# Performance work log

Hardware: AMD Instinct MI355X
Metric: run time of the kernel (lower is better)

## Reference

```python
import jax, jax.numpy as jnp
import numpy as np

B, M, N = 16, 64, 64
F = 64
H2 = 2 * F
L = 2
OUT1, OUT2, PREDS = 32, 32, 256


def skew(x):
    # (b,m,n,c) -> (b,m,m+n-1,c); row i shifted right by i
    b, m, n, c = x.shape
    pad = jnp.pad(x, ((0, 0), (0, 0), (0, m - 1), (0, 0)))
    return jax.vmap(lambda row, r: jnp.roll(row, r, axis=1), in_axes=(1, 0), out_axes=1)(pad, jnp.arange(m))


def unskew(x):
    b, m, n2, c = x.shape
    n = n2 - m + 1
    un = jax.vmap(lambda row, r: jnp.roll(row, -r, axis=1), in_axes=(1, 0), out_axes=1)(x, jnp.arange(m))
    return un[:, :, :n]


def _ln(x, s, b, eps=1e-6):
    mu = jnp.mean(x, axis=-1, keepdims=True)
    var = jnp.mean(jnp.square(x - mu), axis=-1, keepdims=True)
    return (x - mu) * jax.lax.rsqrt(var + eps) * s + b


def _diag_layer(xin, lns, lnb, wis, bis, wss, bss, woc, boc, h0p):
    # xin: (b,m,n2,2F); scan over diagonals (n2 axis)
    b, m, n2, h2 = xin.shape
    f = h2 // 2

    def step(carry, xt):  # xt: (b,m,2F)
        h, c = carry
        xn = _ln(xt, lns, lnb)
        # is_kernel: 1x1 conv == linear; ss_kernel: causal k=2 conv along m
        hprev = jnp.pad(h, ((0, 0), (1, 0), (0, 0)))[:, :-1]
        z = xn @ wis + bis + hprev @ wss[0] + h @ wss[1] + bss  # (b,m,4F)
        fg, ig, og, gg = jnp.split(z, 4, axis=-1)
        cn = jax.nn.sigmoid(fg) * c + jax.nn.sigmoid(ig) * jnp.tanh(gg)
        hn = jax.nn.sigmoid(og) * jnp.tanh(cn)
        x_out = hn @ woc + boc + xn  # residual uses post-LN x (as in source)
        return (hn, cn), x_out

    h0t = jnp.broadcast_to(h0p, (b, m, f))  # h0p: (1,F)
    c0 = jnp.zeros((b, m, f), xin.dtype)
    _, out = jax.lax.scan(step, (h0t, c0), xin.transpose(2, 0, 1, 3))
    return out.transpose(1, 2, 0, 3)


def _forward(im, conv_in_k, conv_in_b, ln_s, ln_b, w_is, b_is, w_ss, b_ss,
             w_oc, b_oc, h0, w_out1, b_out1, w_out2, b_out2, w_head, b_head):
    # mask-A for the 7x7 input conv
    mask = jnp.ones(conv_in_k.shape, conv_in_k.dtype)
    mask = mask.at[3:, 4:].set(0.0)
    mask = mask.at[4:].set(0.0)
    mask = mask.at[3, 3].set(0.0)
    x = skew(im)  # (b,m,n2,1)
    x = jax.lax.conv_general_dilated(x, conv_in_k * mask, (1, 1), 'SAME',
                                     dimension_numbers=('NHWC', 'HWIO', 'NHWC')) + conv_in_b
    b, m, n2, h2 = x.shape
    for l in range(ln_s.shape[0]):
        left = _diag_layer(x, ln_s[l, 0], ln_b[l, 0], w_is[l, 0], b_is[l, 0],
                           w_ss[l, 0], b_ss[l, 0], w_oc[l, 0], b_oc[l, 0], h0[l, 0])
        right = _diag_layer(x[:, :, ::-1, :], ln_s[l, 1], ln_b[l, 1], w_is[l, 1], b_is[l, 1],
                            w_ss[l, 1], b_ss[l, 1], w_oc[l, 1], b_oc[l, 1], h0[l, 1])[:, :, ::-1, :]
        right = jnp.concatenate([jnp.zeros((b, 1, n2, h2), x.dtype), right[:, :-1]], axis=1)
        x = left + right
    x = unskew(x)  # (b,m,n,2F)
    x = x @ w_out1 + b_out1
    x = x @ w_out2 + b_out2
    return x @ w_head + b_head  # (b,m,n,256)


def setup_inputs() -> dict:
    key = jax.random.key(0)
    ks = jax.random.split(key, 10)
    rn = lambda k, s: jax.random.normal(k, s, jnp.float32) * 0.05
    return {
        "im": jax.random.uniform(ks[0], (B, M, N, 1), jnp.float32),
        "conv_in_k": rn(ks[1], (7, 7, 1, H2)),
        "conv_in_b": jnp.zeros((H2,), jnp.float32),
        "ln_s": jnp.ones((L, 2, H2), jnp.float32),
        "ln_b": jnp.zeros((L, 2, H2), jnp.float32),
        "w_is": rn(ks[2], (L, 2, H2, 4 * F)),
        "b_is": jnp.zeros((L, 2, 4 * F), jnp.float32),
        "w_ss": rn(ks[3], (L, 2, 2, F, 4 * F)),
        "b_ss": jnp.zeros((L, 2, 4 * F), jnp.float32),
        "w_oc": rn(ks[4], (L, 2, F, H2)),
        "b_oc": jnp.zeros((L, 2, H2), jnp.float32),
        "h0": rn(ks[5], (L, 2, 1, F)),
        "w_out1": rn(ks[6], (H2, OUT1)),
        "b_out1": jnp.zeros((OUT1,), jnp.float32),
        "w_out2": rn(ks[7], (OUT1, OUT2)),
        "b_out2": jnp.zeros((OUT2,), jnp.float32),
        "w_head": rn(ks[8], (OUT2, PREDS)),
        "b_head": jnp.zeros((PREDS,), jnp.float32),
    }


def reference(im, conv_in_k, conv_in_b, ln_s, ln_b, w_is, b_is, w_ss, b_ss,
              w_oc, b_oc, h0, w_out1, b_out1, w_out2, b_out2, w_head, b_head):
    return _forward(im, conv_in_k, conv_in_b, ln_s, ln_b, w_is, b_is, w_ss, b_ss,
                    w_oc, b_oc, h0, w_out1, b_out1, w_out2, b_out2, w_head, b_head)
```

## Files before the change

### kernel.cpp

```cpp
#include <hip/hip_runtime.h>

typedef unsigned short ushort_t;
typedef unsigned int uint_t;
typedef __attribute__((ext_vector_type(8))) short s8bf;
typedef __attribute__((ext_vector_type(4))) float f32x4;

#define N2 127
#define ACT ((size_t)16*64*127*128)
#define HNE ((size_t)16*64*127*64)
#define MBW ((size_t)32*3*127*64)

__device__ inline float bf_lo(uint_t v){ return __uint_as_float(v << 16); }
__device__ inline float bf_hi(uint_t v){ return __uint_as_float(v & 0xffff0000u); }
__device__ inline ushort_t f2bf(float f){
  uint_t u = __float_as_uint(f);
  uint_t r = ((u >> 16) & 1u) + 0x7fffu;
  return (ushort_t)((u + r) >> 16);
}
__device__ inline float bf2f(ushort_t h){ return __uint_as_float(((uint_t)h) << 16); }
__device__ inline float frcp(float x){ return __builtin_amdgcn_rcpf(x); }
__device__ inline float sigm(float x){ return frcp(1.f + __expf(-x)); }
__device__ inline float tanhf_(float x){
  float e = __expf(2.f * x);
  return 1.f - 2.f * frcp(1.f + e);
}
__device__ inline void unpack8(uint4 u, float* x){
  x[0]=bf_lo(u.x); x[1]=bf_hi(u.x); x[2]=bf_lo(u.y); x[3]=bf_hi(u.y);
  x[4]=bf_lo(u.z); x[5]=bf_hi(u.z); x[6]=bf_lo(u.w); x[7]=bf_hi(u.w);
}
__device__ inline f32x4 zero4(){ f32x4 v; v[0]=0.f; v[1]=0.f; v[2]=0.f; v[3]=0.f; return v; }
__device__ inline f32x4 splat4(float s){ f32x4 v; v[0]=s; v[1]=s; v[2]=s; v[3]=s; return v; }

__device__ inline void rowstats(const float* xr, float& mu, float& rstd){
  float s0=0.f, q0=0.f;
#pragma unroll
  for (int k = 0; k < 32; k++){ s0 += xr[k]; q0 += xr[k]*xr[k]; }
  s0 += __shfl_xor(s0, 1); q0 += __shfl_xor(q0, 1);
  s0 += __shfl_xor(s0, 2); q0 += __shfl_xor(q0, 2);
  mu = s0 * 0.0078125f;
  float var = q0 * 0.0078125f - mu*mu;
  rstd = rsqrtf(var + 1e-6f);
}

__global__ void pack_kernel(const float* __restrict__ w_is, const float* __restrict__ w_ss,
                            const float* __restrict__ b_is, const float* __restrict__ b_ss,
                            const float* __restrict__ w_oc, const float* __restrict__ w1,
                            const float* __restrict__ w2, const float* __restrict__ wh,
                            const float* __restrict__ ck,
                            ushort_t* __restrict__ zWp, ushort_t* __restrict__ wisp,
                            ushort_t* __restrict__ wocp,
                            float* __restrict__ zbias, float* __restrict__ w1T,
                            float* __restrict__ w2T, float* __restrict__ whT,
                            float* __restrict__ kw, uint_t* __restrict__ mb)
{
  int idx = blockIdx.x * 256 + threadIdx.x;
  if (idx < 131072){
    int ld = idx >> 15; int r = idx & 32767;
    int e = r & 7, lane = (r >> 3) & 63, ctg = (r >> 9) & 15, kk = r >> 13;
    int k = kk*32 + ((lane >> 4) & 3)*8 + e;
    int n = ctg*16 + (lane & 15);
    float v;
    if (k < 64) v = w_ss[(((size_t)ld*2 + 0)*64 + k)*256 + n];
    else        v = w_ss[(((size_t)ld*2 + 1)*64 + (k-64))*256 + n];
    zWp[idx] = f2bf(v);
  } else if (idx < 262144){
    int r0 = idx - 131072;
    int ld = r0 >> 15; int r = r0 & 32767;
    int e = r & 7, lane = (r >> 3) & 63, ctg = (r >> 9) & 15, kk = r >> 13;
    int k = kk*32 + ((lane >> 4) & 3)*8 + e;
    int n = ctg*16 + (lane & 15);
    wisp[r0] = f2bf(w_is[((size_t)ld*128 + k)*256 + n]);
  } else if (idx < 294912){
    int r0 = idx - 262144;
    int ld = r0 >> 13; int r = r0 & 8191;
    int e = r & 7, lane = (r >> 3) & 63, ctg = (r >> 9) & 7, kk = (r >> 12) & 1;
    int k = kk*32 + ((lane >> 4) & 3)*8 + e;
    int n = ctg*16 + (lane & 15);
    wocp[r0] = f2bf(w_oc[((size_t)ld*64 + k)*128 + n]);
  } else if (idx < 295936){
    int r = idx - 294912;
    zbias[r] = b_is[r] + b_ss[r];
  } else if (idx < 300032){
    int r = idx - 295936;
    int c = r >> 7, k = r & 127;
    w1T[r] = w1[k*32 + c];
  } else if (idx < 301056){
    int r = idx - 300032;
    int c = r >> 5, k = r & 31;
    w2T[r] = w2[k*32 + c];
  } else if (idx < 309248){
    int r = idx - 301056;
    int o = r >> 5, k = r & 31;
    whT[r] = wh[k*256 + o];
  } else if (idx < 312320){
    int r = idx - 309248;
    int tau = r >> 7, ch = r & 127;
    int di, dj;
    if (tau < 21){ di = tau/7 - 3; dj = tau%7 - 3; } else { di = 0; dj = tau - 24; }
    kw[r] = ck[((di+3)*7 + (dj+3))*128 + ch];
  } else if (idx < (int)(312320 + MBW)){
    mb[idx - 312320] = 0u;
  }
}

__global__ __launch_bounds__(256) void conv_kernel(const float* __restrict__ im,
                const float* __restrict__ cb, const float* __restrict__ kw,
                ushort_t* __restrict__ out)
{
  int tid = threadIdx.x;
  int p = blockIdx.x*2 + (tid >> 7);
  int ch = tid & 127;
  int b = p / (64*N2); int rem = p - b*(64*N2);
  int i = rem / N2; int j = rem - i*N2;
  int base = j - i;
  float acc = cb[ch];
#pragma unroll
  for (int tau = 0; tau < 24; tau++){
    int di = (tau < 21) ? (tau/7 - 3) : 0;
    int dj = (tau < 21) ? (tau%7 - 3) : (tau - 24);
    int ii = i + di;
    int jx = base + dj - di;
    if (ii >= 0 && jx >= 0 && jx < 64)
      acc += im[(b*64 + ii)*64 + jx] * kw[tau*128 + ch];
  }
  out[(size_t)p*128 + ch] = f2bf(acc);
}

__device__ inline void write_frags(const ushort_t* __restrict__ XN,
                                   ushort_t* __restrict__ dst, int tid){
  int lane = tid & 63, kkq = tid >> 6;
  int quad = (lane >> 4) & 3, l16 = lane & 15;
#pragma unroll
  for (int rt = 0; rt < 4; rt++){
    uint4 v = *(const uint4*)&XN[(size_t)(rt*16 + l16)*136 + kkq*32 + quad*8];
    *(uint4*)(dst + (size_t)((kkq*4 + rt)*64 + lane)*8) = v;
  }
}

__device__ inline void ln_to_XN(ushort_t* __restrict__ XN, int row, int lq,
                                const float* xr, float mu, float rstd,
                                const float* __restrict__ ln_s,
                                const float* __restrict__ ln_b, int ld){
#pragma unroll
  for (int k = 0; k < 32; k++){
    int c = lq*32 + k;
    float xn = (xr[k] - mu)*rstd*ln_s[ld*128 + c] + ln_b[ld*128 + c];
    XN[(size_t)row*136 + c] = f2bf(xn);
  }
}

__global__ __launch_bounds__(256, 2) void stage_kernel(
    int mode, int woclyr, int lnlyr,
    ushort_t* __restrict__ Xbuf,
    const ushort_t* __restrict__ hnL, const ushort_t* __restrict__ hnR,
    const ushort_t* __restrict__ wocp, const float* __restrict__ b_oc,
    const float* __restrict__ ln_s, const float* __restrict__ ln_b,
    ushort_t* __restrict__ xnfL, ushort_t* __restrict__ xnfR)
{
  __shared__ __align__(16) float Xout[64*132];
  __shared__ __align__(16) ushort_t XN[64*136];
  __shared__ __align__(16) ushort_t XNh[64*72];

  const int tid = threadIdx.x;
  const int bj = blockIdx.x;
  const int b = bj / 127, j = bj - b*127;
  const int w = tid >> 6, lane = tid & 63, quad = (lane >> 4) & 3, l16 = lane & 15;
  const int row = tid >> 2, lq = tid & 3;

  float xr[32];
  {
    const uint4* p = (const uint4*)(Xbuf + ((size_t)(b*64 + row)*N2 + j)*128 + lq*32);
    unpack8(p[0], xr); unpack8(p[1], xr+8); unpack8(p[2], xr+16); unpack8(p[3], xr+24);
  }
  float mu, rstd;
  rowstats(xr, mu, rstd);

  if (mode == 0){
    ln_to_XN(XN, row, lq, xr, mu, rstd, ln_s, ln_b, lnlyr*2 + 0);
    __syncthreads();
    write_frags(XN, xnfL + (size_t)bj*8192, tid);
    __syncthreads();
    ln_to_XN(XN, row, lq, xr, mu, rstd, ln_s, ln_b, lnlyr*2 + 1);
    __syncthreads();
    write_frags(XN, xnfR + (size_t)bj*8192, tid);
    return;
  }

#pragma unroll 1
  for (int s = 0; s < 2; s++){
    const int ld = woclyr*2 + s;
    ln_to_XN(XN, row, lq, xr, mu, rstd, ln_s, ln_b, ld);
    {
      const ushort_t* hp = s ? hnR : hnL;
      const uint4* p = (const uint4*)(hp + ((size_t)(b*64 + row)*N2 + j)*64 + lq*16);
      *(uint4*)&XNh[(size_t)row*72 + lq*16]     = p[0];
      *(uint4*)&XNh[(size_t)row*72 + lq*16 + 8] = p[1];
    }
    __syncthreads();
    s8bf bw[2][2];
#pragma unroll
    for (int kk = 0; kk < 2; kk++)
#pragma unroll
      for (int jt = 0; jt < 2; jt++)
        bw[kk][jt] = *(const s8bf*)(wocp + (size_t)ld*8192 + (size_t)(((kk*8 + (2*w + jt))*64 + lane)*8));
    f32x4 a2[4][2];
#pragma unroll
    for (int rt = 0; rt < 4; rt++){ a2[rt][0] = zero4(); a2[rt][1] = zero4(); }
#pragma unroll
    for (int kk = 0; kk < 2; kk++)
#pragma unroll
      for (int rt = 0; rt < 4; rt++){
        s8bf a = *(const s8bf*)&XNh[(size_t)(rt*16 + l16)*72 + kk*32 + quad*8];
#pragma unroll
        for (int jt = 0; jt < 2; jt++)
          a2[rt][jt] = __builtin_amdgcn_mfma_f32_16x16x32_bf16(a, bw[kk][jt], a2[rt][jt], 0, 0, 0);
      }
    const float bv0 = b_oc[ld*128 + 32*w + l16];
    const float bv1 = b_oc[ld*128 + 32*w + 16 + l16];
#pragma unroll
    for (int rt = 0; rt < 4; rt++)
#pragma unroll
      for (int jt = 0; jt < 2; jt++){
        int col = 32*w + 16*jt + l16;
        float bv = jt ? bv1 : bv0;
#pragma unroll
        for (int r = 0; r < 4; r++){
          int rr = rt*16 + quad*4 + r;
          float v = a2[rt][jt][r] + bv + bf2f(XN[(size_t)rr*136 + col]);
          if (s == 0) Xout[(size_t)rr*132 + col] = v;
          else if (rr < 63) Xout[(size_t)(rr + 1)*132 + col] += v;
        }
      }
    __syncthreads();
  }

  float xo[32];
#pragma unroll
  for (int k = 0; k < 32; k++) xo[k] = Xout[(size_t)row*132 + lq*32 + k];
  {
    uint_t o[16];
#pragma unroll
    for (int k = 0; k < 16; k++){
      ushort_t lo = f2bf(xo[2*k]);
      ushort_t hi = f2bf(xo[2*k + 1]);
      o[k] = (uint_t)lo | ((uint_t)hi << 16);
    }
    uint4* dst = (uint4*)(Xbuf + ((size_t)(b*64 + row)*N2 + j)*128 + lq*32);
#pragma unroll
    for (int q2 = 0; q2 < 4; q2++) dst[q2] = make_uint4(o[q2*4], o[q2*4+1], o[q2*4+2], o[q2*4+3]);
  }
  if (mode == 2) return;

  float mu2, rstd2;
  rowstats(xo, mu2, rstd2);
  ln_to_XN(XN, row, lq, xo, mu2, rstd2, ln_s, ln_b, lnlyr*2 + 0);
  __syncthreads();
  write_frags(XN, xnfL + (size_t)bj*8192, tid);
  __syncthreads();
  ln_to_XN(XN, row, lq, xo, mu2, rstd2, ln_s, ln_b, lnlyr*2 + 1);
  __syncthreads();
  write_frags(XN, xnfR + (size_t)bj*8192, tid);
}

__global__ __launch_bounds__(256, 1) void diag_kernel(
    const ushort_t* __restrict__ xnfL, const ushort_t* __restrict__ xnfR,
    ushort_t* __restrict__ hnL, ushort_t* __restrict__ hnR,
    const ushort_t* __restrict__ zWp, const ushort_t* __restrict__ wisp,
    const float* __restrict__ zbias, const float* __restrict__ h0, int layer,
    uint_t* __restrict__ mb)
{
  __shared__ ushort_t A[2][16][136];

  const int tid = threadIdx.x;
  const int g = blockIdx.x & 3;
  const int b = (blockIdx.x >> 2) & 15;
  const int d = blockIdx.x >> 6;
  const int ld = layer*2 + d;
  const ushort_t* xnf = d ? xnfR : xnfL;
  ushort_t* hp = d ? hnR : hnL;

  const int w = tid >> 6;
  const int lane = tid & 63;
  const int quad = lane >> 4;
  const int l16 = lane & 15;
  const int cg = w*16 + l16;

  s8bf bss[4][4], bis[4][4];
#pragma unroll
  for (int kk = 0; kk < 4; kk++)
#pragma unroll
    for (int ct = 0; ct < 4; ct++){
      size_t fo = (size_t)(((kk*16 + (w + 4*ct))*64 + lane)*8);
      bss[kk][ct] = *(const s8bf*)(zWp  + (size_t)ld*32768 + fo);
      bis[kk][ct] = *(const s8bf*)(wisp + (size_t)ld*32768 + fo);
    }
  float zb[4];
#pragma unroll
  for (int ct = 0; ct < 4; ct++) zb[ct] = zbias[ld*256 + ct*64 + cg];

  float c_reg[4] = {0.f, 0.f, 0.f, 0.f};

  {
    int r2 = tid >> 4, q8 = tid & 15;
    const float* h0p = h0 + ld*64;
#pragma unroll
    for (int k = 0; k < 8; k++){
      int c = q8*8 + k;
      ushort_t hb = f2bf(h0p[c & 63]);
      ushort_t v;
      if (c < 64) v = (g == 0 && r2 == 0) ? (ushort_t)0 : hb;
      else        v = hb;
      A[0][r2][c] = v;
      A[1][r2][c] = v;
    }
  }

  const int stp8 = d ? -8192 : 8192;
  const ushort_t* xbase = xnf + ((size_t)b*127 + (d ? 126 : 0))*8192;
  uint4 xf[4];
#pragma unroll
  for (int kk = 0; kk < 4; kk++)
    xf[kk] = *(const uint4*)(xbase + (size_t)((kk*4 + g)*64 + lane)*8);

  f32x4 acc[4];
#pragma unroll
  for (int ct = 0; ct < 4; ct++) acc[ct] = splat4(zb[ct]);
#pragma unroll
  for (int kk = 0; kk < 4; kk++){
    s8bf a = *(const s8bf*)&xf[kk];
#pragma unroll
    for (int ct = 0; ct < 4; ct++)
      acc[ct] = __builtin_amdgcn_mfma_f32_16x16x32_bf16(a, bis[kk][ct], acc[ct], 0, 0, 0);
  }
  const ushort_t* pfp = xbase + stp8;
#pragma unroll
  for (int kk = 0; kk < 4; kk++)
    xf[kk] = *(const uint4*)(pfp + (size_t)((kk*4 + g)*64 + lane)*8);
  pfp += stp8;

  const int dj64 = d ? -64 : 64;
  ushort_t* hlane = hp + ((size_t)(b*64 + g*16 + quad*4)*N2 + (d ? 126 : 0))*64 + cg;

  const int bd = b*2 + d;
  uint_t* mbOut = mb + ((size_t)(bd*3 + g)*127)*64;
  const uint_t* mbIn = mb + ((size_t)(bd*3 + (g > 0 ? g - 1 : 0))*127)*64;
  const uint_t stampBase = (uint_t)layer * 127u;
  const bool isProd = (g < 3);
  const bool isCons = (g > 0) && (w == 1);

  __syncthreads();

#pragma unroll 1
  for (int t = 0; t < 127; t++){
    const int pr = t & 1, pn = pr ^ 1;
    const uint_t stamp = stampBase + (uint_t)t + 1u;
    const bool doFetch = isCons && (t < 126);

    uint_t pv = 0;
    if (doFetch)
      pv = __hip_atomic_load(mbIn + (size_t)t*64 + lane,
                             __ATOMIC_RELAXED, __HIP_MEMORY_SCOPE_AGENT);

#pragma unroll
    for (int kk = 0; kk < 4; kk++){
      s8bf af = *(const s8bf*)&A[pr][l16][kk*32 + quad*8];
#pragma unroll
      for (int ct = 0; ct < 4; ct++)
        acc[ct] = __builtin_amdgcn_mfma_f32_16x16x32_bf16(af, bss[kk][ct], acc[ct], 0, 0, 0);
    }

#pragma unroll
    for (int r = 0; r < 4; r++){
      float fg = sigm(acc[0][r]);
      float ig = sigm(acc[1][r]);
      float og = sigm(acc[2][r]);
      float gg = tanhf_(acc[3][r]);
      float cn = fg*c_reg[r] + ig*gg;
      c_reg[r] = cn;
      float hn = og * tanhf_(cn);
      int rr = quad*4 + r;
      ushort_t hb = f2bf(hn);
      A[pn][rr][64 + cg] = hb;
      if (rr < 15) A[pn][rr + 1][cg] = hb;
      hlane[(size_t)r*8128] = hb;
      if (r == 3 && isProd && quad == 3 && t < 126)
        __hip_atomic_store(mbOut + (size_t)t*64 + cg,
                           (stamp << 16) | (uint_t)hb,
                           __ATOMIC_RELAXED, __HIP_MEMORY_SCOPE_AGENT);
    }
    hlane += dj64;

    if (t < 126){
#pragma unroll
      for (int ct = 0; ct < 4; ct++) acc[ct] = splat4(zb[ct]);
#pragma unroll
      for (int kk = 0; kk < 4; kk++){
        s8bf a = *(const s8bf*)&xf[kk];
#pragma unroll
        for (int ct = 0; ct < 4; ct++)
          acc[ct] = __builtin_amdgcn_mfma_f32_16x16x32_bf16(a, bis[kk][ct], acc[ct], 0, 0, 0);
      }
      if (t < 125){
#pragma unroll
        for (int kk = 0; kk < 4; kk++)
          xf[kk] = *(const uint4*)(pfp + (size_t)((kk*4 + g)*64 + lane)*8);
        pfp += stp8;
      }
    }

    if (doFetch){
      while (!__all((pv >> 16) == stamp))
        pv = __hip_atomic_load(mbIn + (size_t)t*64 + lane,
                               __ATOMIC_RELAXED, __HIP_MEMORY_SCOPE_AGENT);
      A[pn][0][lane] = (ushort_t)(pv & 0xffffu);
    }

    __syncthreads();
  }
}

__global__ __launch_bounds__(256) void head_kernel(
    const ushort_t* __restrict__ xfin,
    const float* __restrict__ w1T, const float* __restrict__ b1,
    const float* __restrict__ w2T, const float* __restrict__ b2,
    const float* __restrict__ whT, const float* __restrict__ bh,
    float* __restrict__ out)
{
  __shared__ float xf[64][132];
  __shared__ float v1[64][36];
  __shared__ float v2[64][36];
  int tid = threadIdx.x;
  int b = blockIdx.x >> 6, i = blockIdx.x & 63;
  {
    int jj = tid >> 2, q = tid & 3;
    size_t base = ((size_t)(b*64 + i)*N2 + (i + jj))*128 + q*32;
    const uint4* pL = (const uint4*)(xfin + base);
    float x[32];
    unpack8(pL[0], x); unpack8(pL[1], x+8); unpack8(pL[2], x+16); unpack8(pL[3], x+24);
#pragma unroll
    for (int k = 0; k < 32; k++) xf[jj][q*32 + k] = x[k];
  }
  __syncthreads();
  {
    int c1 = tid & 31, jg = tid >> 5;
    float wr[128];
    const float4* wp = (const float4*)(w1T + c1*128);
#pragma unroll
    for (int kk = 0; kk < 32; kk++) ((float4*)wr)[kk] = wp[kk];
#pragma unroll 1
    for (int jj2 = 0; jj2 < 8; jj2++){
      int jr = jg*8 + jj2;
      float a0=0.f,a1=0.f,a2=0.f,a3=0.f;
#pragma unroll
      for (int kk = 0; kk < 32; kk++){
        float4 xv = *(const float4*)&xf[jr][kk*4];
        a0 += xv.x*wr[kk*4]; a1 += xv.y*wr[kk*4+1]; a2 += xv.z*wr[kk*4+2]; a3 += xv.w*wr[kk*4+3];
      }
      v1[jr][c1] = b1[c1] + (a0+a1)+(a2+a3);
    }
  }
  __syncthreads();
  {
    int c2 = tid & 31, jg = tid >> 5;
    float wr[32];
    const float4* wp = (const float4*)(w2T + c2*32);
#pragma unroll
    for (int kk = 0; kk < 8; kk++) ((float4*)wr)[kk] = wp[kk];
#pragma unroll 1
    for (int jj2 = 0; jj2 < 8; jj2++){
      int jr = jg*8 + jj2;
      float a0=0.f,a1=0.f,a2=0.f,a3=0.f;
#pragma unroll
      for (int kk = 0; kk < 8; kk++){
        float4 xv = *(const float4*)&v1[jr][kk*4];
        a0 += xv.x*wr[kk*4]; a1 += xv.y*wr[kk*4+1]; a2 += xv.z*wr[kk*4+2]; a3 += xv.w*wr[kk*4+3];
      }
      v2[jr][c2] = b2[c2] + (a0+a1)+(a2+a3);
    }
  }
  __syncthreads();
  {
    int o = tid;
    float wr[32];
    const float4* wp = (const float4*)(whT + o*32);
#pragma unroll
    for (int kk = 0; kk < 8; kk++) ((float4*)wr)[kk] = wp[kk];
    float bo = bh[o];
#pragma unroll 1
    for (int jr = 0; jr < 64; jr++){
      float a0=0.f,a1=0.f,a2=0.f,a3=0.f;
#pragma unroll
      for (int kk = 0; kk < 8; kk++){
        float4 xv = *(const float4*)&v2[jr][kk*4];
        a0 += xv.x*wr[kk*4]; a1 += xv.y*wr[kk*4+1]; a2 += xv.z*wr[kk*4+2]; a3 += xv.w*wr[kk*4+3];
      }
      out[(((size_t)b*64 + i)*64 + jr)*256 + o] = bo + (a0+a1)+(a2+a3);
    }
  }
}

extern "C" void kernel_launch(void* const* d_in, const int* in_sizes, int n_in,
                              void* d_out, int out_size, void* d_ws, size_t ws_size,
                              hipStream_t stream)
{
  const float* im   = (const float*)d_in[0];
  const float* ck   = (const float*)d_in[1];
  const float* cb   = (const float*)d_in[2];
  const float* ln_s = (const float*)d_in[3];
  const float* ln_b = (const float*)d_in[4];
  const float* w_is = (const float*)d_in[5];
  const float* b_is = (const float*)d_in[6];
  const float* w_ss = (const float*)d_in[7];
  const float* b_ss = (const float*)d_in[8];
  const float* w_oc = (const float*)d_in[9];
  const float* b_oc = (const float*)d_in[10];
  const float* h0   = (const float*)d_in[11];
  const float* w1   = (const float*)d_in[12];
  const float* b1   = (const float*)d_in[13];
  const float* w2   = (const float*)d_in[14];
  const float* b2   = (const float*)d_in[15];
  const float* wh   = (const float*)d_in[16];
  const float* bh   = (const float*)d_in[17];

  ushort_t* Xbuf = (ushort_t*)d_ws;
  ushort_t* xnfL = Xbuf + ACT;
  ushort_t* xnfR = xnfL + ACT;
  ushort_t* hnL  = xnfR + ACT;
  ushort_t* hnR  = hnL + HNE;
  ushort_t* zWp  = hnR + HNE;
  ushort_t* wisp = zWp + 131072;
  ushort_t* wocp = wisp + 131072;
  float* zbias = (float*)(wocp + 32768);
  float* w1T   = zbias + 1024;
  float* w2T   = w1T + 4096;
  float* whT   = w2T + 1024;
  float* kw    = whT + 8192;
  uint_t* mb   = (uint_t*)d_out;

  pack_kernel<<<4268, 256, 0, stream>>>(w_is, w_ss, b_is, b_ss, w_oc, w1, w2, wh, ck,
                                        zWp, wisp, wocp, zbias, w1T, w2T, whT, kw, mb);
  conv_kernel<<<65024, 256, 0, stream>>>(im, cb, kw, Xbuf);
  stage_kernel<<<2032, 256, 0, stream>>>(0, 0, 0, Xbuf, nullptr, nullptr,
                                         wocp, b_oc, ln_s, ln_b, xnfL, xnfR);
  diag_kernel<<<128, 256, 0, stream>>>(xnfL, xnfR, hnL, hnR, zWp, wisp, zbias, h0, 0, mb);
  stage_kernel<<<2032, 256, 0, stream>>>(1, 0, 1, Xbuf, hnL, hnR,
                                         wocp, b_oc, ln_s, ln_b, xnfL, xnfR);
  diag_kernel<<<128, 256, 0, stream>>>(xnfL, xnfR, hnL, hnR, zWp, wisp, zbias, h0, 1, mb);
  stage_kernel<<<2032, 256, 0, stream>>>(2, 1, 0, Xbuf, hnL, hnR,
                                         wocp, b_oc, ln_s, ln_b, xnfL, xnfR);
  head_kernel<<<1024, 256, 0, stream>>>(Xbuf, w1T, b1, w2T, b2, whT, bh, (float*)d_out);
}
```

Before: 793.6 us.

## Merge both scan directions into one 512-thread diag block and deepen prefetch

```diff
diff --git a/kernel.cpp b/kernel.cpp
--- a/kernel.cpp
+++ b/kernel.cpp
@@ -262,24 +262,25 @@
   write_frags(XN, xnfR + (size_t)bj*8192, tid);
 }
 
-__global__ __launch_bounds__(256, 1) void diag_kernel(
+__global__ __launch_bounds__(512, 1) void diag_kernel(
     const ushort_t* __restrict__ xnfL, const ushort_t* __restrict__ xnfR,
     ushort_t* __restrict__ hnL, ushort_t* __restrict__ hnR,
     const ushort_t* __restrict__ zWp, const ushort_t* __restrict__ wisp,
     const float* __restrict__ zbias, const float* __restrict__ h0, int layer,
     uint_t* __restrict__ mb)
 {
-  __shared__ ushort_t A[2][16][136];
+  __shared__ ushort_t A[2][2][16][136];
 
   const int tid = threadIdx.x;
   const int g = blockIdx.x & 3;
-  const int b = (blockIdx.x >> 2) & 15;
-  const int d = blockIdx.x >> 6;
+  const int b = blockIdx.x >> 2;
+  const int w8 = tid >> 6;
+  const int d = w8 >> 2;
+  const int w = w8 & 3;
   const int ld = layer*2 + d;
   const ushort_t* xnf = d ? xnfR : xnfL;
   ushort_t* hp = d ? hnR : hnL;
 
-  const int w = tid >> 6;
   const int lane = tid & 63;
   const int quad = lane >> 4;
   const int l16 = lane & 15;
@@ -301,7 +302,8 @@
   float c_reg[4] = {0.f, 0.f, 0.f, 0.f};
 
   {
-    int r2 = tid >> 4, q8 = tid & 15;
+    int t8 = tid & 255;
+    int r2 = t8 >> 4, q8 = t8 & 15;
     const float* h0p = h0 + ld*64;
 #pragma unroll
     for (int k = 0; k < 8; k++){
@@ -310,33 +312,41 @@
       ushort_t v;
       if (c < 64) v = (g == 0 && r2 == 0) ? (ushort_t)0 : hb;
       else        v = hb;
-      A[0][r2][c] = v;
-      A[1][r2][c] = v;
+      A[d][0][r2][c] = v;
+      A[d][1][r2][c] = v;
     }
   }
 
   const int stp8 = d ? -8192 : 8192;
   const ushort_t* xbase = xnf + ((size_t)b*127 + (d ? 126 : 0))*8192;
-  uint4 xf[4];
-#pragma unroll
-  for (int kk = 0; kk < 4; kk++)
-    xf[kk] = *(const uint4*)(xbase + (size_t)((kk*4 + g)*64 + lane)*8);
-
   f32x4 acc[4];
-#pragma unroll
-  for (int ct = 0; ct < 4; ct++) acc[ct] = splat4(zb[ct]);
-#pragma unroll
-  for (int kk = 0; kk < 4; kk++){
-    s8bf a = *(const s8bf*)&xf[kk];
-#pragma unroll
-    for (int ct = 0; ct < 4; ct++)
-      acc[ct] = __builtin_amdgcn_mfma_f32_16x16x32_bf16(a, bis[kk][ct], acc[ct], 0, 0, 0);
-  }
-  const ushort_t* pfp = xbase + stp8;
-#pragma unroll
-  for (int kk = 0; kk < 4; kk++)
-    xf[kk] = *(const uint4*)(pfp + (size_t)((kk*4 + g)*64 + lane)*8);
-  pfp += stp8;
+  {
+    uint4 xf0[4];
+#pragma unroll
+    for (int kk = 0; kk < 4; kk++)
+      xf0[kk] = *(const uint4*)(xbase + (size_t)((kk*4 + g)*64 + lane)*8);
+#pragma unroll
+    for (int ct = 0; ct < 4; ct++) acc[ct] = splat4(zb[ct]);
+#pragma unroll
+    for (int kk = 0; kk < 4; kk++){
+      s8bf a = *(const s8bf*)&xf0[kk];
+#pragma unroll
+      for (int ct = 0; ct < 4; ct++)
+        acc[ct] = __builtin_amdgcn_mfma_f32_16x16x32_bf16(a, bis[kk][ct], acc[ct], 0, 0, 0);
+    }
+  }
+  uint4 xfA[4], xfB[4];
+  {
+    const ushort_t* p1 = xbase + stp8;
+    const ushort_t* p2 = xbase + 2*stp8;
+#pragma unroll
+    for (int kk = 0; kk < 4; kk++)
+      xfA[kk] = *(const uint4*)(p1 + (size_t)((kk*4 + g)*64 + lane)*8);
+#pragma unroll
+    for (int kk = 0; kk < 4; kk++)
+      xfB[kk] = *(const uint4*)(p2 + (size_t)((kk*4 + g)*64 + lane)*8);
+  }
+  const ushort_t* pfp = xbase + 3*stp8;
 
   const int dj64 = d ? -64 : 64;
   ushort_t* hlane = hp + ((size_t)(b*64 + g*16 + quad*4)*N2 + (d ? 126 : 0))*64 + cg;
@@ -363,7 +373,7 @@
 
 #pragma unroll
     for (int kk = 0; kk < 4; kk++){
-      s8bf af = *(const s8bf*)&A[pr][l16][kk*32 + quad*8];
+      s8bf af = *(const s8bf*)&A[d][pr][l16][kk*32 + quad*8];
 #pragma unroll
       for (int ct = 0; ct < 4; ct++)
         acc[ct] = __builtin_amdgcn_mfma_f32_16x16x32_bf16(af, bss[kk][ct], acc[ct], 0, 0, 0);
@@ -380,8 +390,8 @@
       float hn = og * tanhf_(cn);
       int rr = quad*4 + r;
       ushort_t hb = f2bf(hn);
-      A[pn][rr][64 + cg] = hb;
-      if (rr < 15) A[pn][rr + 1][cg] = hb;
+      A[d][pn][rr][64 + cg] = hb;
+      if (rr < 15) A[d][pn][rr + 1][cg] = hb;
       hlane[(size_t)r*8128] = hb;
       if (r == 3 && isProd && quad == 3 && t < 126)
         __hip_atomic_store(mbOut + (size_t)t*64 + cg,
@@ -395,15 +405,17 @@
       for (int ct = 0; ct < 4; ct++) acc[ct] = splat4(zb[ct]);
 #pragma unroll
       for (int kk = 0; kk < 4; kk++){
-        s8bf a = *(const s8bf*)&xf[kk];
+        s8bf a = *(const s8bf*)&xfA[kk];
 #pragma unroll
         for (int ct = 0; ct < 4; ct++)
           acc[ct] = __builtin_amdgcn_mfma_f32_16x16x32_bf16(a, bis[kk][ct], acc[ct], 0, 0, 0);
       }
-      if (t < 125){
+#pragma unroll
+      for (int kk = 0; kk < 4; kk++) xfA[kk] = xfB[kk];
+      if (t < 124){
 #pragma unroll
         for (int kk = 0; kk < 4; kk++)
-          xf[kk] = *(const uint4*)(pfp + (size_t)((kk*4 + g)*64 + lane)*8);
+          xfB[kk] = *(const uint4*)(pfp + (size_t)((kk*4 + g)*64 + lane)*8);
         pfp += stp8;
       }
     }
@@ -412,7 +424,7 @@
       while (!__all((pv >> 16) == stamp))
         pv = __hip_atomic_load(mbIn + (size_t)t*64 + lane,
                                __ATOMIC_RELAXED, __HIP_MEMORY_SCOPE_AGENT);
-      A[pn][0][lane] = (ushort_t)(pv & 0xffffu);
+      A[d][pn][0][lane] = (ushort_t)(pv & 0xffffu);
     }
 
     __syncthreads();
@@ -542,10 +554,10 @@
   conv_kernel<<<65024, 256, 0, stream>>>(im, cb, kw, Xbuf);
   stage_kernel<<<2032, 256, 0, stream>>>(0, 0, 0, Xbuf, nullptr, nullptr,
                                          wocp, b_oc, ln_s, ln_b, xnfL, xnfR);
-  diag_kernel<<<128, 256, 0, stream>>>(xnfL, xnfR, hnL, hnR, zWp, wisp, zbias, h0, 0, mb);
+  diag_kernel<<<64, 512, 0, stream>>>(xnfL, xnfR, hnL, hnR, zWp, wisp, zbias, h0, 0, mb);
   stage_kernel<<<2032, 256, 0, stream>>>(1, 0, 1, Xbuf, hnL, hnR,
                                          wocp, b_oc, ln_s, ln_b, xnfL, xnfR);
-  diag_kernel<<<128, 256, 0, stream>>>(xnfL, xnfR, hnL, hnR, zWp, wisp, zbias, h0, 1, mb);
+  diag_kernel<<<64, 512, 0, stream>>>(xnfL, xnfR, hnL, hnR, zWp, wisp, zbias, h0, 1, mb);
   stage_kernel<<<2032, 256, 0, stream>>>(2, 1, 0, Xbuf, hnL, hnR,
                                          wocp, b_oc, ln_s, ln_b, xnfL, xnfR);
   head_kernel<<<1024, 256, 0, stream>>>(Xbuf, w1T, b1, w2T, b2, whT, bh, (float*)d_out);
```

After: 885.6 us. 11.6% more time.

## Deepen input prefetch to two steps and relax per-step barrier waitcnt

Applied to the files above, without the earlier changes.

```diff
diff --git a/kernel.cpp b/kernel.cpp
--- a/kernel.cpp
+++ b/kernel.cpp
@@ -317,26 +317,34 @@
 
   const int stp8 = d ? -8192 : 8192;
   const ushort_t* xbase = xnf + ((size_t)b*127 + (d ? 126 : 0))*8192;
-  uint4 xf[4];
-#pragma unroll
-  for (int kk = 0; kk < 4; kk++)
-    xf[kk] = *(const uint4*)(xbase + (size_t)((kk*4 + g)*64 + lane)*8);
-
   f32x4 acc[4];
-#pragma unroll
-  for (int ct = 0; ct < 4; ct++) acc[ct] = splat4(zb[ct]);
-#pragma unroll
-  for (int kk = 0; kk < 4; kk++){
-    s8bf a = *(const s8bf*)&xf[kk];
-#pragma unroll
-    for (int ct = 0; ct < 4; ct++)
-      acc[ct] = __builtin_amdgcn_mfma_f32_16x16x32_bf16(a, bis[kk][ct], acc[ct], 0, 0, 0);
-  }
-  const ushort_t* pfp = xbase + stp8;
-#pragma unroll
-  for (int kk = 0; kk < 4; kk++)
-    xf[kk] = *(const uint4*)(pfp + (size_t)((kk*4 + g)*64 + lane)*8);
-  pfp += stp8;
+  {
+    uint4 xf0[4];
+#pragma unroll
+    for (int kk = 0; kk < 4; kk++)
+      xf0[kk] = *(const uint4*)(xbase + (size_t)((kk*4 + g)*64 + lane)*8);
+#pragma unroll
+    for (int ct = 0; ct < 4; ct++) acc[ct] = splat4(zb[ct]);
+#pragma unroll
+    for (int kk = 0; kk < 4; kk++){
+      s8bf a = *(const s8bf*)&xf0[kk];
+#pragma unroll
+      for (int ct = 0; ct < 4; ct++)
+        acc[ct] = __builtin_amdgcn_mfma_f32_16x16x32_bf16(a, bis[kk][ct], acc[ct], 0, 0, 0);
+    }
+  }
+  uint4 xfA[4], xfB[4];
+  {
+    const ushort_t* p1 = xbase + stp8;
+    const ushort_t* p2 = xbase + 2*stp8;
+#pragma unroll
+    for (int kk = 0; kk < 4; kk++)
+      xfA[kk] = *(const uint4*)(p1 + (size_t)((kk*4 + g)*64 + lane)*8);
+#pragma unroll
+    for (int kk = 0; kk < 4; kk++)
+      xfB[kk] = *(const uint4*)(p2 + (size_t)((kk*4 + g)*64 + lane)*8);
+  }
+  const ushort_t* pfp = xbase + 3*stp8;
 
   const int dj64 = d ? -64 : 64;
   ushort_t* hlane = hp + ((size_t)(b*64 + g*16 + quad*4)*N2 + (d ? 126 : 0))*64 + cg;
@@ -395,15 +403,17 @@
       for (int ct = 0; ct < 4; ct++) acc[ct] = splat4(zb[ct]);
 #pragma unroll
       for (int kk = 0; kk < 4; kk++){
-        s8bf a = *(const s8bf*)&xf[kk];
+        s8bf a = *(const s8bf*)&xfA[kk];
 #pragma unroll
         for (int ct = 0; ct < 4; ct++)
           acc[ct] = __builtin_amdgcn_mfma_f32_16x16x32_bf16(a, bis[kk][ct], acc[ct], 0, 0, 0);
       }
-      if (t < 125){
+#pragma unroll
+      for (int kk = 0; kk < 4; kk++) xfA[kk] = xfB[kk];
+      if (t < 124){
 #pragma unroll
         for (int kk = 0; kk < 4; kk++)
-          xf[kk] = *(const uint4*)(pfp + (size_t)((kk*4 + g)*64 + lane)*8);
+          xfB[kk] = *(const uint4*)(pfp + (size_t)((kk*4 + g)*64 + lane)*8);
         pfp += stp8;
       }
     }
@@ -415,7 +425,10 @@
       A[pn][0][lane] = (ushort_t)(pv & 0xffffu);
     }
 
-    __syncthreads();
+    __builtin_amdgcn_sched_barrier(0);
+    asm volatile("s_waitcnt lgkmcnt(0)" ::: "memory");
+    __builtin_amdgcn_s_barrier();
+    __builtin_amdgcn_sched_barrier(0);
   }
 }
 
```

Measured after the change: 808.9 us. Within noise of the previous version (+1.9%).

## Merge row-group pairs into one 512-thread block to cut cross-block handoffs

Applied to the files above, without the earlier changes.

```diff
diff --git a/kernel.cpp b/kernel.cpp
--- a/kernel.cpp
+++ b/kernel.cpp
@@ -8,7 +8,7 @@
 #define N2 127
 #define ACT ((size_t)16*64*127*128)
 #define HNE ((size_t)16*64*127*64)
-#define MBW ((size_t)32*3*127*64)
+#define MBW ((size_t)32*127*64)
 
 __device__ inline float bf_lo(uint_t v){ return __uint_as_float(v << 16); }
 __device__ inline float bf_hi(uint_t v){ return __uint_as_float(v & 0xffff0000u); }
@@ -262,24 +262,28 @@
   write_frags(XN, xnfR + (size_t)bj*8192, tid);
 }
 
-__global__ __launch_bounds__(256, 1) void diag_kernel(
+__global__ __launch_bounds__(512, 1) void diag_kernel(
     const ushort_t* __restrict__ xnfL, const ushort_t* __restrict__ xnfR,
     ushort_t* __restrict__ hnL, ushort_t* __restrict__ hnR,
     const ushort_t* __restrict__ zWp, const ushort_t* __restrict__ wisp,
     const float* __restrict__ zbias, const float* __restrict__ h0, int layer,
     uint_t* __restrict__ mb)
 {
-  __shared__ ushort_t A[2][16][136];
+  __shared__ ushort_t A[2][2][16][136];
 
   const int tid = threadIdx.x;
-  const int g = blockIdx.x & 3;
-  const int b = (blockIdx.x >> 2) & 15;
-  const int d = blockIdx.x >> 6;
+  const int chain = blockIdx.x & 31;
+  const int gp = blockIdx.x >> 5;
+  const int b = chain & 15;
+  const int d = chain >> 4;
+  const int w8 = tid >> 6;
+  const int sub = w8 >> 2;
+  const int w = w8 & 3;
+  const int g = gp*2 + sub;
   const int ld = layer*2 + d;
   const ushort_t* xnf = d ? xnfR : xnfL;
   ushort_t* hp = d ? hnR : hnL;
 
-  const int w = tid >> 6;
   const int lane = tid & 63;
   const int quad = lane >> 4;
   const int l16 = lane & 15;
@@ -301,7 +305,8 @@
   float c_reg[4] = {0.f, 0.f, 0.f, 0.f};
 
   {
-    int r2 = tid >> 4, q8 = tid & 15;
+    int t8 = tid & 255;
+    int r2 = t8 >> 4, q8 = t8 & 15;
     const float* h0p = h0 + ld*64;
 #pragma unroll
     for (int k = 0; k < 8; k++){
@@ -310,8 +315,8 @@
       ushort_t v;
       if (c < 64) v = (g == 0 && r2 == 0) ? (ushort_t)0 : hb;
       else        v = hb;
-      A[0][r2][c] = v;
-      A[1][r2][c] = v;
+      A[sub][0][r2][c] = v;
+      A[sub][1][r2][c] = v;
     }
   }
 
@@ -341,12 +346,10 @@
   const int dj64 = d ? -64 : 64;
   ushort_t* hlane = hp + ((size_t)(b*64 + g*16 + quad*4)*N2 + (d ? 126 : 0))*64 + cg;
 
-  const int bd = b*2 + d;
-  uint_t* mbOut = mb + ((size_t)(bd*3 + g)*127)*64;
-  const uint_t* mbIn = mb + ((size_t)(bd*3 + (g > 0 ? g - 1 : 0))*127)*64;
+  uint_t* mbl = mb + (size_t)chain*127*64;
   const uint_t stampBase = (uint_t)layer * 127u;
-  const bool isProd = (g < 3);
-  const bool isCons = (g > 0) && (w == 1);
+  const bool isProd = (gp == 0 && sub == 1);
+  const bool isCons = (gp == 1 && sub == 0 && w == 1);
 
   __syncthreads();
 
@@ -358,19 +361,24 @@
 
     uint_t pv = 0;
     if (doFetch)
-      pv = __hip_atomic_load(mbIn + (size_t)t*64 + lane,
+      pv = __hip_atomic_load(mbl + (size_t)t*64 + lane,
                              __ATOMIC_RELAXED, __HIP_MEMORY_SCOPE_AGENT);
 
 #pragma unroll
     for (int kk = 0; kk < 4; kk++){
-      s8bf af = *(const s8bf*)&A[pr][l16][kk*32 + quad*8];
+      s8bf af = *(const s8bf*)&A[sub][pr][l16][kk*32 + quad*8];
 #pragma unroll
       for (int ct = 0; ct < 4; ct++)
         acc[ct] = __builtin_amdgcn_mfma_f32_16x16x32_bf16(af, bss[kk][ct], acc[ct], 0, 0, 0);
     }
 
-#pragma unroll
-    for (int r = 0; r < 4; r++){
+    if (doFetch && (pv >> 16) != stamp)
+      pv = __hip_atomic_load(mbl + (size_t)t*64 + lane,
+                             __ATOMIC_RELAXED, __HIP_MEMORY_SCOPE_AGENT);
+
+#pragma unroll
+    for (int ri = 0; ri < 4; ri++){
+      const int r = (ri == 0) ? 3 : ri - 1;
       float fg = sigm(acc[0][r]);
       float ig = sigm(acc[1][r]);
       float og = sigm(acc[2][r]);
@@ -380,11 +388,12 @@
       float hn = og * tanhf_(cn);
       int rr = quad*4 + r;
       ushort_t hb = f2bf(hn);
-      A[pn][rr][64 + cg] = hb;
-      if (rr < 15) A[pn][rr + 1][cg] = hb;
+      A[sub][pn][rr][64 + cg] = hb;
+      if (rr < 15)          A[sub][pn][rr + 1][cg] = hb;
+      else if (sub == 0)    A[1][pn][0][cg] = hb;
       hlane[(size_t)r*8128] = hb;
-      if (r == 3 && isProd && quad == 3 && t < 126)
-        __hip_atomic_store(mbOut + (size_t)t*64 + cg,
+      if (ri == 0 && isProd && quad == 3 && t < 126)
+        __hip_atomic_store(mbl + (size_t)t*64 + cg,
                            (stamp << 16) | (uint_t)hb,
                            __ATOMIC_RELAXED, __HIP_MEMORY_SCOPE_AGENT);
     }
@@ -410,9 +419,9 @@
 
     if (doFetch){
       while (!__all((pv >> 16) == stamp))
-        pv = __hip_atomic_load(mbIn + (size_t)t*64 + lane,
+        pv = __hip_atomic_load(mbl + (size_t)t*64 + lane,
                                __ATOMIC_RELAXED, __HIP_MEMORY_SCOPE_AGENT);
-      A[pn][0][lane] = (ushort_t)(pv & 0xffffu);
+      A[0][pn][0][lane] = (ushort_t)(pv & 0xffffu);
     }
 
     __syncthreads();
@@ -537,15 +546,15 @@
   float* kw    = whT + 8192;
   uint_t* mb   = (uint_t*)d_out;
 
-  pack_kernel<<<4268, 256, 0, stream>>>(w_is, w_ss, b_is, b_ss, w_oc, w1, w2, wh, ck,
+  pack_kernel<<<2236, 256, 0, stream>>>(w_is, w_ss, b_is, b_ss, w_oc, w1, w2, wh, ck,
                                         zWp, wisp, wocp, zbias, w1T, w2T, whT, kw, mb);
   conv_kernel<<<65024, 256, 0, stream>>>(im, cb, kw, Xbuf);
   stage_kernel<<<2032, 256, 0, stream>>>(0, 0, 0, Xbuf, nullptr, nullptr,
                                          wocp, b_oc, ln_s, ln_b, xnfL, xnfR);
-  diag_kernel<<<128, 256, 0, stream>>>(xnfL, xnfR, hnL, hnR, zWp, wisp, zbias, h0, 0, mb);
+  diag_kernel<<<64, 512, 0, stream>>>(xnfL, xnfR, hnL, hnR, zWp, wisp, zbias, h0, 0, mb);
   stage_kernel<<<2032, 256, 0, stream>>>(1, 0, 1, Xbuf, hnL, hnR,
                                          wocp, b_oc, ln_s, ln_b, xnfL, xnfR);
-  diag_kernel<<<128, 256, 0, stream>>>(xnfL, xnfR, hnL, hnR, zWp, wisp, zbias, h0, 1, mb);
+  diag_kernel<<<64, 512, 0, stream>>>(xnfL, xnfR, hnL, hnR, zWp, wisp, zbias, h0, 1, mb);
   stage_kernel<<<2032, 256, 0, stream>>>(2, 1, 0, Xbuf, hnL, hnR,
                                          wocp, b_oc, ln_s, ln_b, xnfL, xnfR);
   head_kernel<<<1024, 256, 0, stream>>>(Xbuf, w1T, b1, w2T, b2, whT, bh, (float*)d_out);
```

Result: slower. 819.8 us (+3.3%).
